# Performance work log

Measured on AMD Instinct MI355X. Metric: run time of the kernel, lower is better.

The kernel has to match this reference:

```python
import jax, jax.numpy as jnp
import numpy as np

N_NODES = 40000
N_EDGES = 640000
D_FEAT = 128
HIDDEN = 128
N_CLASSES = 10
N_GRAPHS = 64


def setup_inputs() -> dict:
    key = jax.random.key(0)
    ks = jax.random.split(key, 8)
    x = jax.random.normal(ks[0], (N_NODES, D_FEAT), dtype=jnp.float32)
    edge_index = jax.random.randint(ks[1], (2, N_EDGES), 0, N_NODES, dtype=jnp.int32)
    batch = jnp.sort(jax.random.randint(ks[2], (N_NODES,), 0, N_GRAPHS, dtype=jnp.int32))
    s1 = 1.0 / np.sqrt(D_FEAT)
    s2 = 1.0 / np.sqrt(HIDDEN)
    W1 = jax.random.normal(ks[3], (D_FEAT, HIDDEN), dtype=jnp.float32) * s1
    b1 = jnp.zeros((HIDDEN,), dtype=jnp.float32)
    W2 = jax.random.normal(ks[4], (HIDDEN, HIDDEN), dtype=jnp.float32) * s2
    b2 = jnp.zeros((HIDDEN,), dtype=jnp.float32)
    lin_w = jax.random.normal(ks[5], (HIDDEN, N_CLASSES), dtype=jnp.float32) * s2
    lin_b = jnp.zeros((N_CLASSES,), dtype=jnp.float32)
    return {"x": x, "edge_index": edge_index, "batch": batch,
            "W1": W1, "b1": b1, "W2": W2, "b2": b2,
            "lin_w": lin_w, "lin_b": lin_b}


def _gcn_conv(x, src, dst, norm, W, b, n_nodes):
    # x' = D^-1/2 (A + I) D^-1/2 (x W) + b ; self-loops already in src/dst/norm
    xw = x @ W                                   # [N, H]
    msg = xw[src] * norm[:, None]                # gather + scale  [E+N, H]
    out = jax.ops.segment_sum(msg, dst, num_segments=n_nodes)  # scatter-add
    return out + b


def reference(x, edge_index, batch, W1, b1, W2, b2, lin_w, lin_b):
    n_nodes = x.shape[0]
    loop = jnp.arange(n_nodes, dtype=edge_index.dtype)
    src = jnp.concatenate([edge_index[0], loop])  # add self-loops (fill=1)
    dst = jnp.concatenate([edge_index[1], loop])
    deg = jax.ops.segment_sum(jnp.ones_like(src, dtype=x.dtype), dst,
                              num_segments=n_nodes)
    dinv = jnp.where(deg > 0, jax.lax.rsqrt(jnp.maximum(deg, 1e-12)), 0.0)
    norm = dinv[src] * dinv[dst]

    h = jax.nn.relu(_gcn_conv(x, src, dst, norm, W1, b1, n_nodes))
    h = jax.nn.relu(_gcn_conv(h, src, dst, norm, W2, b2, n_nodes))

    # global average pooling per graph
    sums = jax.ops.segment_sum(h, batch, num_segments=N_GRAPHS)      # [B, H]
    cnt = jax.ops.segment_sum(jnp.ones((n_nodes,), x.dtype), batch,
                              num_segments=N_GRAPHS)
    pooled = sums / jnp.maximum(cnt, 1.0)[:, None]

    logits = pooled @ lin_w + lin_b                                  # [B, K]
    return logits
```

## Files before the change

kernel.cpp:

```cpp
#include <hip/hip_runtime.h>
#include <stdint.h>

#define N_NODES 40000
#define N_EDGES 640000
#define HID 128
#define NGRAPH 64
#define NCLASS 10
#define CAP 64
#define POISON ((int)0xAAAAAAAAu)
#define ZROW 40000

typedef unsigned short u16;
typedef unsigned char u8;
typedef __attribute__((ext_vector_type(8))) short bf16x8;
typedef __attribute__((ext_vector_type(4))) float f32x4;
typedef __attribute__((ext_vector_type(2))) float f32x2;

static __device__ __forceinline__ u16 f2bf(float f) {
    union { float f; uint32_t i; } v; v.f = f;
    uint32_t u = v.i;
    u = (u + 0x7fff + ((u >> 16) & 1)) >> 16;
    return (u16)u;
}

static __device__ __forceinline__ void acc_row(uint2 p, float* a) {
    f32x2 f01 = __builtin_amdgcn_cvt_pk_f32_fp8((int)p.x, false);
    f32x2 f23 = __builtin_amdgcn_cvt_pk_f32_fp8((int)p.x, true);
    f32x2 f45 = __builtin_amdgcn_cvt_pk_f32_fp8((int)p.y, false);
    f32x2 f67 = __builtin_amdgcn_cvt_pk_f32_fp8((int)p.y, true);
    a[0] += f01[0]; a[1] += f01[1]; a[2] += f23[0]; a[3] += f23[1];
    a[4] += f45[0]; a[5] += f45[1]; a[6] += f67[0]; a[7] += f67[1];
}

static __device__ __forceinline__ void agg_gather_pad(const u8* __restrict__ base,
        const u16* __restrict__ csr, int e, int e1, float* a) {
    int sc[6]; uint2 pc[6];
    #pragma unroll
    for (int u = 0; u < 6; ++u) sc[u] = (int)csr[e + u];
    #pragma unroll
    for (int u = 0; u < 6; ++u) pc[u] = *(const uint2*)(base + (size_t)sc[u] * HID);
    e += 6;
    while (e < e1) {
        int sn[6]; uint2 pn[6];
        #pragma unroll
        for (int u = 0; u < 6; ++u) sn[u] = (int)csr[e + u];
        #pragma unroll
        for (int u = 0; u < 6; ++u) pn[u] = *(const uint2*)(base + (size_t)sn[u] * HID);
        #pragma unroll
        for (int u = 0; u < 6; ++u) acc_row(pc[u], a);
        #pragma unroll
        for (int u = 0; u < 6; ++u) pc[u] = pn[u];
        e += 6;
    }
    #pragma unroll
    for (int u = 0; u < 6; ++u) acc_row(pc[u], a);
}

static __device__ __forceinline__ int padded_deg(int deg) {
    int degp = ((deg + 5) / 6) * 6;
    if (degp < 6) degp = 6;
    if (degp > 60) degp = 60;
    return degp;
}

__launch_bounds__(256)
__global__ void k_fill_wprep(const int* __restrict__ srcs, const int* __restrict__ dsts,
                             int* __restrict__ cursor, u16* __restrict__ csr,
                             const float* __restrict__ W1, const float* __restrict__ W2,
                             u16* __restrict__ wswz1, u16* __restrict__ wswz2) {
    if (blockIdx.x < 2500) {
        int e = blockIdx.x * 256 + threadIdx.x;
        int s = srcs[e], d = dsts[e];
        int old = atomicAdd(&cursor[d], 1);
        int slot = old - POISON;
        if (slot < CAP) csr[(d << 6) + slot] = (u16)s;
    } else {
        int gid = (blockIdx.x - 2500) * 256 + threadIdx.x;
        int idx = gid & 16383;
        const float* W = (gid < 16384) ? W1 : W2;
        u16* o = (gid < 16384) ? wswz1 : wswz2;
        int j = idx & 7;
        int frag = idx >> 3;
        int l = frag & 63;
        int ks = (frag >> 6) & 3;
        int nt = frag >> 8;
        int k = ks * 32 + (l >> 4) * 8 + j;
        int n = nt * 16 + (l & 15);
        o[idx] = f2bf(W[k * HID + n]);
    }
}

__launch_bounds__(256)
__global__ void k_gemm1(const float* __restrict__ x, const u16* __restrict__ wswz1,
                        const int* __restrict__ cursor, u8* __restrict__ z1,
                        u16* __restrict__ csr) {
    __shared__ u16 wlds[16384];
    int t = threadIdx.x;
    if (blockIdx.x >= 625) {
        if (blockIdx.x == 625 && t < 16)
            *(uint2*)(z1 + (size_t)ZROW * HID + t * 8) = make_uint2(0u, 0u);
        int nid = (blockIdx.x - 625) * 256 + t;
        if (nid < N_NODES) {
            int deg = cursor[nid] - POISON;
            int degp = padded_deg(deg);
            for (int s = deg; s < degp; ++s) csr[(nid << 6) + s] = (u16)ZROW;
        }
        return;
    }
    {
        const uint4* s4 = (const uint4*)wswz1;
        uint4* d4 = (uint4*)wlds;
        #pragma unroll
        for (int i = 0; i < 8; ++i) d4[t + 256 * i] = s4[t + 256 * i];
    }
    __syncthreads();
    int lane = t & 63, wv = t >> 6;
    int quad = lane >> 4, m15 = lane & 15;
    int strip = blockIdx.x * 4 + wv;
    int m0 = strip * 16;
    float dv[4];
    #pragma unroll
    for (int r = 0; r < 4; ++r)
        dv[r] = rsqrtf((float)(cursor[m0 + quad * 4 + r] - POISON + 1));
    bf16x8 af[4];
    const float* arow = x + (size_t)(m0 + m15) * HID;
    #pragma unroll
    for (int ks = 0; ks < 4; ++ks) {
        float4 u = *(const float4*)(arow + ks * 32 + quad * 8);
        float4 v = *(const float4*)(arow + ks * 32 + quad * 8 + 4);
        bf16x8 f;
        f[0] = (short)f2bf(u.x); f[1] = (short)f2bf(u.y);
        f[2] = (short)f2bf(u.z); f[3] = (short)f2bf(u.w);
        f[4] = (short)f2bf(v.x); f[5] = (short)f2bf(v.y);
        f[6] = (short)f2bf(v.z); f[7] = (short)f2bf(v.w);
        af[ks] = f;
    }
    #pragma unroll
    for (int nt = 0; nt < 8; ++nt) {
        f32x4 acc = {0.f, 0.f, 0.f, 0.f};
        #pragma unroll
        for (int ks = 0; ks < 4; ++ks) {
            bf16x8 bfr = *(const bf16x8*)(&wlds[((nt * 4 + ks) * 64 + lane) * 8]);
            acc = __builtin_amdgcn_mfma_f32_16x16x32_bf16(af[ks], bfr, acc, 0, 0, 0);
        }
        #pragma unroll
        for (int r = 0; r < 4; ++r) {
            float zc = acc[r] * dv[r];
            int pk = __builtin_amdgcn_cvt_pk_fp8_f32(zc, zc, 0, false);
            z1[(size_t)(m0 + quad * 4 + r) * HID + nt * 16 + m15] = (u8)pk;
        }
    }
}

__launch_bounds__(256, 8)
__global__ void k_agg_gemm(const u8* __restrict__ zin, const int* __restrict__ cursor,
                           const u16* __restrict__ csr, const float* __restrict__ bias,
                           const u16* __restrict__ wswz2, u8* __restrict__ zout) {
    __shared__ u16 htile[16 * 136];
    int t = threadIdx.x;
    if (blockIdx.x == 0 && t < 16)
        *(uint2*)(zout + (size_t)ZROW * HID + t * 8) = make_uint2(0u, 0u);
    int lane = t & 63, wv = t >> 6;
    int q = lane >> 4, sub = lane & 15;
    int i = blockIdx.x * 16 + wv * 4 + q;
    int deg = cursor[i] - POISON;
    int degp = padded_deg(deg);
    float di = rsqrtf((float)(deg + 1));
    const u8* base = zin + (size_t)sub * 8;
    uint2 ps = *(const uint2*)(base + (size_t)i * HID);
    float a[8];
    {
        f32x2 t0 = __builtin_amdgcn_cvt_pk_f32_fp8((int)ps.x, false);
        f32x2 t1 = __builtin_amdgcn_cvt_pk_f32_fp8((int)ps.x, true);
        f32x2 t2 = __builtin_amdgcn_cvt_pk_f32_fp8((int)ps.y, false);
        f32x2 t3 = __builtin_amdgcn_cvt_pk_f32_fp8((int)ps.y, true);
        a[0] = t0[0]; a[1] = t0[1]; a[2] = t1[0]; a[3] = t1[1];
        a[4] = t2[0]; a[5] = t2[1]; a[6] = t3[0]; a[7] = t3[1];
    }
    int e = i << 6;
    agg_gather_pad(base, csr, e, e + degp, a);

    float4 b0 = *(const float4*)(bias + sub * 8);
    float4 b1v = *(const float4*)(bias + sub * 8 + 4);
    float r0 = fmaxf(di * a[0] + b0.x, 0.f),  r1 = fmaxf(di * a[1] + b0.y, 0.f);
    float r2 = fmaxf(di * a[2] + b0.z, 0.f),  r3 = fmaxf(di * a[3] + b0.w, 0.f);
    float r4 = fmaxf(di * a[4] + b1v.x, 0.f), r5 = fmaxf(di * a[5] + b1v.y, 0.f);
    float r6 = fmaxf(di * a[6] + b1v.z, 0.f), r7 = fmaxf(di * a[7] + b1v.w, 0.f);
    int nl = wv * 4 + q;
    uint4 o;
    o.x = (uint32_t)f2bf(r0) | ((uint32_t)f2bf(r1) << 16);
    o.y = (uint32_t)f2bf(r2) | ((uint32_t)f2bf(r3) << 16);
    o.z = (uint32_t)f2bf(r4) | ((uint32_t)f2bf(r5) << 16);
    o.w = (uint32_t)f2bf(r6) | ((uint32_t)f2bf(r7) << 16);
    *(uint4*)(&htile[nl * 136 + sub * 8]) = o;
    __syncthreads();

    int quad = q, m15 = sub;
    bf16x8 af[4];
    #pragma unroll
    for (int ks = 0; ks < 4; ++ks)
        af[ks] = *(const bf16x8*)(&htile[m15 * 136 + ks * 32 + quad * 8]);
    int m0 = blockIdx.x * 16;
    float dv[4];
    #pragma unroll
    for (int r = 0; r < 4; ++r)
        dv[r] = rsqrtf((float)(cursor[m0 + quad * 4 + r] - POISON + 1));
    #pragma unroll
    for (int n2 = 0; n2 < 2; ++n2) {
        int nt = wv * 2 + n2;
        f32x4 acc = {0.f, 0.f, 0.f, 0.f};
        #pragma unroll
        for (int ks = 0; ks < 4; ++ks) {
            bf16x8 bfr = *(const bf16x8*)(wswz2 + ((nt * 4 + ks) * 64 + lane) * 8);
            acc = __builtin_amdgcn_mfma_f32_16x16x32_bf16(af[ks], bfr, acc, 0, 0, 0);
        }
        #pragma unroll
        for (int r = 0; r < 4; ++r) {
            float zc = acc[r] * dv[r];
            int pk = __builtin_amdgcn_cvt_pk_fp8_f32(zc, zc, 0, false);
            zout[(size_t)(m0 + quad * 4 + r) * HID + nt * 16 + m15] = (u8)pk;
        }
    }
}

__launch_bounds__(256, 8)
__global__ void k_agg2pool(const u8* __restrict__ zin, const int* __restrict__ cursor,
                           const u16* __restrict__ csr, const float* __restrict__ bias,
                           const int* __restrict__ batch, float* __restrict__ gpool) {
    __shared__ float hf[16 * 132];
    __shared__ int sbatch[16];
    int t = threadIdx.x;
    int lane = t & 63, wv = t >> 6;
    int q = lane >> 4, sub = lane & 15;
    int i = blockIdx.x * 16 + wv * 4 + q;
    if (t < 16) sbatch[t] = batch[blockIdx.x * 16 + t];
    int deg = cursor[i] - POISON;
    int degp = padded_deg(deg);
    float di = rsqrtf((float)(deg + 1));
    const u8* base = zin + (size_t)sub * 8;
    uint2 ps = *(const uint2*)(base + (size_t)i * HID);
    float a[8];
    {
        f32x2 t0 = __builtin_amdgcn_cvt_pk_f32_fp8((int)ps.x, false);
        f32x2 t1 = __builtin_amdgcn_cvt_pk_f32_fp8((int)ps.x, true);
        f32x2 t2 = __builtin_amdgcn_cvt_pk_f32_fp8((int)ps.y, false);
        f32x2 t3 = __builtin_amdgcn_cvt_pk_f32_fp8((int)ps.y, true);
        a[0] = t0[0]; a[1] = t0[1]; a[2] = t1[0]; a[3] = t1[1];
        a[4] = t2[0]; a[5] = t2[1]; a[6] = t3[0]; a[7] = t3[1];
    }
    int e = i << 6;
    agg_gather_pad(base, csr, e, e + degp, a);

    float4 b0 = *(const float4*)(bias + sub * 8);
    float4 b1v = *(const float4*)(bias + sub * 8 + 4);
    int nl = wv * 4 + q;
    float* hrow = &hf[nl * 132 + sub * 8];
    float4 o0, o1;
    o0.x = fmaxf(di * a[0] + b0.x, 0.f);  o0.y = fmaxf(di * a[1] + b0.y, 0.f);
    o0.z = fmaxf(di * a[2] + b0.z, 0.f);  o0.w = fmaxf(di * a[3] + b0.w, 0.f);
    o1.x = fmaxf(di * a[4] + b1v.x, 0.f); o1.y = fmaxf(di * a[5] + b1v.y, 0.f);
    o1.z = fmaxf(di * a[6] + b1v.z, 0.f); o1.w = fmaxf(di * a[7] + b1v.w, 0.f);
    *(float4*)hrow = o0;
    *(float4*)(hrow + 4) = o1;
    __syncthreads();

    if (t < HID) {
        float s = 0.f;
        int gcur = sbatch[0];
        #pragma unroll
        for (int j = 0; j < 16; ++j) {
            int gj = sbatch[j];
            if (gj != gcur) {
                atomicAdd(&gpool[gcur * HID + t], s);
                s = 0.f;
                gcur = gj;
            }
            s += hf[j * 132 + t];
        }
        atomicAdd(&gpool[gcur * HID + t], s);
    }
}

__launch_bounds__(128)
__global__ void k_pool2(const float* __restrict__ gpool, const int* __restrict__ batch,
                        const float* __restrict__ lin_w, const float* __restrict__ lin_b,
                        float* __restrict__ outp) {
    __shared__ float sh[HID];
    int g = blockIdx.x;
    int t = threadIdx.x;
    int lo = 0, n = N_NODES;
    while (n > 0) { int half = n >> 1; int mid = lo + half;
        if (batch[mid] < g) { lo = mid + 1; n -= half + 1; } else n = half; }
    int hi = lo, n2 = N_NODES - lo;
    while (n2 > 0) { int half = n2 >> 1; int mid = hi + half;
        if (batch[mid] < g + 1) { hi = mid + 1; n2 -= half + 1; } else n2 = half; }
    float c = fmaxf((float)(hi - lo), 1.f);
    sh[t] = gpool[g * HID + t] / c;
    __syncthreads();
    if (t < NCLASS) {
        float a = lin_b[t];
        #pragma unroll 8
        for (int f = 0; f < HID; ++f)
            a += sh[f] * lin_w[f * NCLASS + t];
        outp[g * NCLASS + t] = a;
    }
}

extern "C" void kernel_launch(void* const* d_in, const int* in_sizes, int n_in,
                              void* d_out, int out_size, void* d_ws, size_t ws_size,
                              hipStream_t stream) {
    const float* x    = (const float*)d_in[0];
    const int* eidx   = (const int*)d_in[1];
    const int* batch  = (const int*)d_in[2];
    const float* W1   = (const float*)d_in[3];
    const float* b1   = (const float*)d_in[4];
    const float* W2   = (const float*)d_in[5];
    const float* b2   = (const float*)d_in[6];
    const float* lw   = (const float*)d_in[7];
    const float* lb   = (const float*)d_in[8];
    float* out = (float*)d_out;

    char* ws = (char*)d_ws;
    int*   cursor  = (int*)(ws + 0);
    float* gpool   = (float*)(ws + 160000);
    u16*   csr     = (u16*)(ws + 192768);
    u16*   wswz1   = (u16*)(ws + 5312768);
    u16*   wswz2   = (u16*)(ws + 5345536);
    u8*    bufZ1   = (u8*)(ws + 5378304);
    u8*    bufZ2   = (u8*)(ws + 10498432);

    const int* src = eidx;
    const int* dst = eidx + N_EDGES;

    k_fill_wprep<<<2628, 256, 0, stream>>>(src, dst, cursor, csr, W1, W2, wswz1, wswz2);
    k_gemm1<<<782, 256, 0, stream>>>(x, wswz1, cursor, bufZ1, csr);
    k_agg_gemm<<<2500, 256, 0, stream>>>(bufZ1, cursor, csr, b1,
                                         wswz2, bufZ2);
    k_agg2pool<<<2500, 256, 0, stream>>>(bufZ2, cursor, csr, b2,
                                         batch, gpool);
    k_pool2<<<NGRAPH, 128, 0, stream>>>(gpool, batch, lw, lb, out);
}
```

Measured before the change: 158.4 us.

## Split feature rows into XCD-pinned halves and separate layer-2 aggregation from GEMM

The fp8 node-feature buffers are re-laid out as two 64-byte column halves with separate row ranges. Each aggregation block handles one half, chosen from blockIdx modulo 8, so that four XCDs gather only from one half and their L2 caches hold a smaller working set. The fused layer-1 aggregate+GEMM kernel is split into k_agg1, which writes bf16 h1 to global memory, and a new k_gemm2 that stages W2 in LDS. The aim is better L2 hit rates on the random gathers, at the cost of an extra global round trip for h1, one more launch, and twice as many blocks each doing half the work per row.

```diff
diff --git a/kernel.cpp b/kernel.cpp
--- a/kernel.cpp
+++ b/kernel.cpp
@@ -9,6 +9,7 @@
 #define CAP 64
 #define POISON ((int)0xAAAAAAAAu)
 #define ZROW 40000
+#define RSTRIDE 40001
 
 typedef unsigned short u16;
 typedef unsigned char u8;
@@ -23,37 +24,34 @@
     return (u16)u;
 }
 
-static __device__ __forceinline__ void acc_row(uint2 p, float* a) {
-    f32x2 f01 = __builtin_amdgcn_cvt_pk_f32_fp8((int)p.x, false);
-    f32x2 f23 = __builtin_amdgcn_cvt_pk_f32_fp8((int)p.x, true);
-    f32x2 f45 = __builtin_amdgcn_cvt_pk_f32_fp8((int)p.y, false);
-    f32x2 f67 = __builtin_amdgcn_cvt_pk_f32_fp8((int)p.y, true);
+static __device__ __forceinline__ void acc_row4(uint32_t p, float* a) {
+    f32x2 f01 = __builtin_amdgcn_cvt_pk_f32_fp8((int)p, false);
+    f32x2 f23 = __builtin_amdgcn_cvt_pk_f32_fp8((int)p, true);
     a[0] += f01[0]; a[1] += f01[1]; a[2] += f23[0]; a[3] += f23[1];
-    a[4] += f45[0]; a[5] += f45[1]; a[6] += f67[0]; a[7] += f67[1];
-}
-
-static __device__ __forceinline__ void agg_gather_pad(const u8* __restrict__ base,
+}
+
+static __device__ __forceinline__ void agg_gather_pad4(const u8* __restrict__ lb,
         const u16* __restrict__ csr, int e, int e1, float* a) {
-    int sc[6]; uint2 pc[6];
+    int sc[6]; uint32_t pc[6];
     #pragma unroll
     for (int u = 0; u < 6; ++u) sc[u] = (int)csr[e + u];
     #pragma unroll
-    for (int u = 0; u < 6; ++u) pc[u] = *(const uint2*)(base + (size_t)sc[u] * HID);
+    for (int u = 0; u < 6; ++u) pc[u] = *(const uint32_t*)(lb + (size_t)sc[u] * 64);
     e += 6;
     while (e < e1) {
-        int sn[6]; uint2 pn[6];
+        int sn[6]; uint32_t pn[6];
         #pragma unroll
         for (int u = 0; u < 6; ++u) sn[u] = (int)csr[e + u];
         #pragma unroll
-        for (int u = 0; u < 6; ++u) pn[u] = *(const uint2*)(base + (size_t)sn[u] * HID);
-        #pragma unroll
-        for (int u = 0; u < 6; ++u) acc_row(pc[u], a);
+        for (int u = 0; u < 6; ++u) pn[u] = *(const uint32_t*)(lb + (size_t)sn[u] * 64);
+        #pragma unroll
+        for (int u = 0; u < 6; ++u) acc_row4(pc[u], a);
         #pragma unroll
         for (int u = 0; u < 6; ++u) pc[u] = pn[u];
         e += 6;
     }
     #pragma unroll
-    for (int u = 0; u < 6; ++u) acc_row(pc[u], a);
+    for (int u = 0; u < 6; ++u) acc_row4(pc[u], a);
 }
 
 static __device__ __forceinline__ int padded_deg(int deg) {
@@ -97,8 +95,11 @@
     __shared__ u16 wlds[16384];
     int t = threadIdx.x;
     if (blockIdx.x >= 625) {
-        if (blockIdx.x == 625 && t < 16)
-            *(uint2*)(z1 + (size_t)ZROW * HID + t * 8) = make_uint2(0u, 0u);
+        if (blockIdx.x == 625 && t < 16) {
+            int hh = t >> 3;
+            *(uint2*)(z1 + ((size_t)(hh * RSTRIDE + ZROW)) * 64 + (t & 7) * 8)
+                = make_uint2(0u, 0u);
+        }
         int nid = (blockIdx.x - 625) * 256 + t;
         if (nid < N_NODES) {
             int deg = cursor[nid] - POISON;
@@ -147,78 +148,93 @@
         for (int r = 0; r < 4; ++r) {
             float zc = acc[r] * dv[r];
             int pk = __builtin_amdgcn_cvt_pk_fp8_f32(zc, zc, 0, false);
-            z1[(size_t)(m0 + quad * 4 + r) * HID + nt * 16 + m15] = (u8)pk;
+            int node = m0 + quad * 4 + r;
+            z1[((size_t)((nt >> 2) * RSTRIDE + node)) * 64 + (nt & 3) * 16 + m15] = (u8)pk;
         }
     }
 }
 
 __launch_bounds__(256, 8)
-__global__ void k_agg_gemm(const u8* __restrict__ zin, const int* __restrict__ cursor,
-                           const u16* __restrict__ csr, const float* __restrict__ bias,
-                           const u16* __restrict__ wswz2, u8* __restrict__ zout) {
-    __shared__ u16 htile[16 * 136];
-    int t = threadIdx.x;
-    if (blockIdx.x == 0 && t < 16)
-        *(uint2*)(zout + (size_t)ZROW * HID + t * 8) = make_uint2(0u, 0u);
+__global__ void k_agg1(const u8* __restrict__ zin, const int* __restrict__ cursor,
+                       const u16* __restrict__ csr, const float* __restrict__ bias,
+                       u16* __restrict__ h1) {
+    int t = threadIdx.x;
+    int bid = blockIdx.x;
+    int xcd = bid & 7;
+    int half = xcd >> 2;
+    int s = (bid >> 3) * 4 + (xcd & 3);
     int lane = t & 63, wv = t >> 6;
-    int q = lane >> 4, sub = lane & 15;
-    int i = blockIdx.x * 16 + wv * 4 + q;
+    int q = lane >> 4, L = lane & 15;
+    int i = s * 16 + wv * 4 + q;
     int deg = cursor[i] - POISON;
     int degp = padded_deg(deg);
     float di = rsqrtf((float)(deg + 1));
-    const u8* base = zin + (size_t)sub * 8;
-    uint2 ps = *(const uint2*)(base + (size_t)i * HID);
-    float a[8];
+    const u8* lb = zin + (size_t)(half * RSTRIDE) * 64 + L * 4;
+    uint32_t ps = *(const uint32_t*)(lb + (size_t)i * 64);
+    float a[4];
     {
-        f32x2 t0 = __builtin_amdgcn_cvt_pk_f32_fp8((int)ps.x, false);
-        f32x2 t1 = __builtin_amdgcn_cvt_pk_f32_fp8((int)ps.x, true);
-        f32x2 t2 = __builtin_amdgcn_cvt_pk_f32_fp8((int)ps.y, false);
-        f32x2 t3 = __builtin_amdgcn_cvt_pk_f32_fp8((int)ps.y, true);
-        a[0] = t0[0]; a[1] = t0[1]; a[2] = t1[0]; a[3] = t1[1];
-        a[4] = t2[0]; a[5] = t2[1]; a[6] = t3[0]; a[7] = t3[1];
+        f32x2 f01 = __builtin_amdgcn_cvt_pk_f32_fp8((int)ps, false);
+        f32x2 f23 = __builtin_amdgcn_cvt_pk_f32_fp8((int)ps, true);
+        a[0] = f01[0]; a[1] = f01[1]; a[2] = f23[0]; a[3] = f23[1];
     }
     int e = i << 6;
-    agg_gather_pad(base, csr, e, e + degp, a);
-
-    float4 b0 = *(const float4*)(bias + sub * 8);
-    float4 b1v = *(const float4*)(bias + sub * 8 + 4);
-    float r0 = fmaxf(di * a[0] + b0.x, 0.f),  r1 = fmaxf(di * a[1] + b0.y, 0.f);
-    float r2 = fmaxf(di * a[2] + b0.z, 0.f),  r3 = fmaxf(di * a[3] + b0.w, 0.f);
-    float r4 = fmaxf(di * a[4] + b1v.x, 0.f), r5 = fmaxf(di * a[5] + b1v.y, 0.f);
-    float r6 = fmaxf(di * a[6] + b1v.z, 0.f), r7 = fmaxf(di * a[7] + b1v.w, 0.f);
-    int nl = wv * 4 + q;
-    uint4 o;
+    agg_gather_pad4(lb, csr, e, e + degp, a);
+    float4 b = *(const float4*)(bias + half * 64 + L * 4);
+    float r0 = fmaxf(di * a[0] + b.x, 0.f), r1 = fmaxf(di * a[1] + b.y, 0.f);
+    float r2 = fmaxf(di * a[2] + b.z, 0.f), r3 = fmaxf(di * a[3] + b.w, 0.f);
+    uint2 o;
     o.x = (uint32_t)f2bf(r0) | ((uint32_t)f2bf(r1) << 16);
     o.y = (uint32_t)f2bf(r2) | ((uint32_t)f2bf(r3) << 16);
-    o.z = (uint32_t)f2bf(r4) | ((uint32_t)f2bf(r5) << 16);
-    o.w = (uint32_t)f2bf(r6) | ((uint32_t)f2bf(r7) << 16);
-    *(uint4*)(&htile[nl * 136 + sub * 8]) = o;
+    *(uint2*)(h1 + ((size_t)(half * N_NODES + i)) * 64 + L * 4) = o;
+}
+
+__launch_bounds__(256)
+__global__ void k_gemm2(const u16* __restrict__ h1, const u16* __restrict__ wswz2,
+                        const int* __restrict__ cursor, u8* __restrict__ z2) {
+    __shared__ u16 wlds[16384];
+    int t = threadIdx.x;
+    {
+        const uint4* s4 = (const uint4*)wswz2;
+        uint4* d4 = (uint4*)wlds;
+        #pragma unroll
+        for (int i = 0; i < 8; ++i) d4[t + 256 * i] = s4[t + 256 * i];
+    }
+    if (blockIdx.x == 0 && t < 16) {
+        int hh = t >> 3;
+        *(uint2*)(z2 + ((size_t)(hh * RSTRIDE + ZROW)) * 64 + (t & 7) * 8)
+            = make_uint2(0u, 0u);
+    }
     __syncthreads();
-
-    int quad = q, m15 = sub;
-    bf16x8 af[4];
-    #pragma unroll
-    for (int ks = 0; ks < 4; ++ks)
-        af[ks] = *(const bf16x8*)(&htile[m15 * 136 + ks * 32 + quad * 8]);
-    int m0 = blockIdx.x * 16;
+    int lane = t & 63, wv = t >> 6;
+    int quad = lane >> 4, m15 = lane & 15;
+    int strip = blockIdx.x * 4 + wv;
+    int m0 = strip * 16;
     float dv[4];
     #pragma unroll
     for (int r = 0; r < 4; ++r)
         dv[r] = rsqrtf((float)(cursor[m0 + quad * 4 + r] - POISON + 1));
-    #pragma unroll
-    for (int n2 = 0; n2 < 2; ++n2) {
-        int nt = wv * 2 + n2;
+    bf16x8 af[4];
+    int node = m0 + m15;
+    #pragma unroll
+    for (int ks = 0; ks < 4; ++ks) {
+        int f = ks * 32 + quad * 8;
+        int hh = f >> 6, fo = f & 63;
+        af[ks] = *(const bf16x8*)(h1 + ((size_t)(hh * N_NODES + node)) * 64 + fo);
+    }
+    #pragma unroll
+    for (int nt = 0; nt < 8; ++nt) {
         f32x4 acc = {0.f, 0.f, 0.f, 0.f};
         #pragma unroll
         for (int ks = 0; ks < 4; ++ks) {
-            bf16x8 bfr = *(const bf16x8*)(wswz2 + ((nt * 4 + ks) * 64 + lane) * 8);
+            bf16x8 bfr = *(const bf16x8*)(&wlds[((nt * 4 + ks) * 64 + lane) * 8]);
             acc = __builtin_amdgcn_mfma_f32_16x16x32_bf16(af[ks], bfr, acc, 0, 0, 0);
         }
         #pragma unroll
         for (int r = 0; r < 4; ++r) {
             float zc = acc[r] * dv[r];
             int pk = __builtin_amdgcn_cvt_pk_fp8_f32(zc, zc, 0, false);
-            zout[(size_t)(m0 + quad * 4 + r) * HID + nt * 16 + m15] = (u8)pk;
+            int nd = m0 + quad * 4 + r;
+            z2[((size_t)((nt >> 2) * RSTRIDE + nd)) * 64 + (nt & 3) * 16 + m15] = (u8)pk;
         }
     }
 }
@@ -227,57 +243,54 @@
 __global__ void k_agg2pool(const u8* __restrict__ zin, const int* __restrict__ cursor,
                            const u16* __restrict__ csr, const float* __restrict__ bias,
                            const int* __restrict__ batch, float* __restrict__ gpool) {
-    __shared__ float hf[16 * 132];
+    __shared__ float hf[16 * 68];
     __shared__ int sbatch[16];
     int t = threadIdx.x;
+    int bid = blockIdx.x;
+    int xcd = bid & 7;
+    int half = xcd >> 2;
+    int s = (bid >> 3) * 4 + (xcd & 3);
+    if (t < 16) sbatch[t] = batch[s * 16 + t];
     int lane = t & 63, wv = t >> 6;
-    int q = lane >> 4, sub = lane & 15;
-    int i = blockIdx.x * 16 + wv * 4 + q;
-    if (t < 16) sbatch[t] = batch[blockIdx.x * 16 + t];
+    int q = lane >> 4, L = lane & 15;
+    int i = s * 16 + wv * 4 + q;
     int deg = cursor[i] - POISON;
     int degp = padded_deg(deg);
     float di = rsqrtf((float)(deg + 1));
-    const u8* base = zin + (size_t)sub * 8;
-    uint2 ps = *(const uint2*)(base + (size_t)i * HID);
-    float a[8];
+    const u8* lb = zin + (size_t)(half * RSTRIDE) * 64 + L * 4;
+    uint32_t ps = *(const uint32_t*)(lb + (size_t)i * 64);
+    float a[4];
     {
-        f32x2 t0 = __builtin_amdgcn_cvt_pk_f32_fp8((int)ps.x, false);
-        f32x2 t1 = __builtin_amdgcn_cvt_pk_f32_fp8((int)ps.x, true);
-        f32x2 t2 = __builtin_amdgcn_cvt_pk_f32_fp8((int)ps.y, false);
-        f32x2 t3 = __builtin_amdgcn_cvt_pk_f32_fp8((int)ps.y, true);
-        a[0] = t0[0]; a[1] = t0[1]; a[2] = t1[0]; a[3] = t1[1];
-        a[4] = t2[0]; a[5] = t2[1]; a[6] = t3[0]; a[7] = t3[1];
+        f32x2 f01 = __builtin_amdgcn_cvt_pk_f32_fp8((int)ps, false);
+        f32x2 f23 = __builtin_amdgcn_cvt_pk_f32_fp8((int)ps, true);
+        a[0] = f01[0]; a[1] = f01[1]; a[2] = f23[0]; a[3] = f23[1];
     }
     int e = i << 6;
-    agg_gather_pad(base, csr, e, e + degp, a);
-
-    float4 b0 = *(const float4*)(bias + sub * 8);
-    float4 b1v = *(const float4*)(bias + sub * 8 + 4);
+    agg_gather_pad4(lb, csr, e, e + degp, a);
+    float4 b = *(const float4*)(bias + half * 64 + L * 4);
     int nl = wv * 4 + q;
-    float* hrow = &hf[nl * 132 + sub * 8];
-    float4 o0, o1;
-    o0.x = fmaxf(di * a[0] + b0.x, 0.f);  o0.y = fmaxf(di * a[1] + b0.y, 0.f);
-    o0.z = fmaxf(di * a[2] + b0.z, 0.f);  o0.w = fmaxf(di * a[3] + b0.w, 0.f);
-    o1.x = fmaxf(di * a[4] + b1v.x, 0.f); o1.y = fmaxf(di * a[5] + b1v.y, 0.f);
-    o1.z = fmaxf(di * a[6] + b1v.z, 0.f); o1.w = fmaxf(di * a[7] + b1v.w, 0.f);
-    *(float4*)hrow = o0;
-    *(float4*)(hrow + 4) = o1;
+    float4 o;
+    o.x = fmaxf(di * a[0] + b.x, 0.f);
+    o.y = fmaxf(di * a[1] + b.y, 0.f);
+    o.z = fmaxf(di * a[2] + b.z, 0.f);
+    o.w = fmaxf(di * a[3] + b.w, 0.f);
+    *(float4*)(&hf[nl * 68 + L * 4]) = o;
     __syncthreads();
 
-    if (t < HID) {
-        float s = 0.f;
+    if (t < 64) {
+        float ssum = 0.f;
         int gcur = sbatch[0];
         #pragma unroll
         for (int j = 0; j < 16; ++j) {
             int gj = sbatch[j];
             if (gj != gcur) {
-                atomicAdd(&gpool[gcur * HID + t], s);
-                s = 0.f;
+                atomicAdd(&gpool[gcur * HID + half * 64 + t], ssum);
+                ssum = 0.f;
                 gcur = gj;
             }
-            s += hf[j * 132 + t];
-        }
-        atomicAdd(&gpool[gcur * HID + t], s);
+            ssum += hf[j * 68 + t];
+        }
+        atomicAdd(&gpool[gcur * HID + half * 64 + t], ssum);
     }
 }
 
@@ -327,16 +340,17 @@
     u16*   wswz1   = (u16*)(ws + 5312768);
     u16*   wswz2   = (u16*)(ws + 5345536);
     u8*    bufZ1   = (u8*)(ws + 5378304);
-    u8*    bufZ2   = (u8*)(ws + 10498432);
+    u16*   h1      = (u16*)(ws + 10498432);
+    u8*    bufZ2   = (u8*)(ws + 20738432);
 
     const int* src = eidx;
     const int* dst = eidx + N_EDGES;
 
     k_fill_wprep<<<2628, 256, 0, stream>>>(src, dst, cursor, csr, W1, W2, wswz1, wswz2);
     k_gemm1<<<782, 256, 0, stream>>>(x, wswz1, cursor, bufZ1, csr);
-    k_agg_gemm<<<2500, 256, 0, stream>>>(bufZ1, cursor, csr, b1,
-                                         wswz2, bufZ2);
-    k_agg2pool<<<2500, 256, 0, stream>>>(bufZ2, cursor, csr, b2,
+    k_agg1<<<5000, 256, 0, stream>>>(bufZ1, cursor, csr, b1, h1);
+    k_gemm2<<<625, 256, 0, stream>>>(h1, wswz2, cursor, bufZ2);
+    k_agg2pool<<<5000, 256, 0, stream>>>(bufZ2, cursor, csr, b2,
                                          batch, gpool);
     k_pool2<<<NGRAPH, 128, 0, stream>>>(gpool, batch, lw, lb, out);
 }
```

Measured after the change: 162.7 us. +2.7%, slower.

## Partition edges into destination buckets before building CSR

Applied to the files above, without the earlier changes.

Replaces the direct per-edge atomic CSR fill with two passes. The first bins edges by destination block of 512 nodes using shared-memory counters plus one global atomic per bucket per block. The second kernel walks each bucket and does the per-destination atomics and CSR writes, so those accesses stay within a localized address range. This aims to reduce scattered global atomics and cache misses, at the cost of an extra kernel launch and an intermediate buffer round trip. It relies on the workspace being poison-initialized for gbcur, and on BCAP being large enough for each bucket.

```diff
diff --git a/kernel.cpp b/kernel.cpp
--- a/kernel.cpp
+++ b/kernel.cpp
@@ -9,6 +9,8 @@
 #define CAP 64
 #define POISON ((int)0xAAAAAAAAu)
 #define ZROW 40000
+#define NBKT 80
+#define BCAP 12288
 
 typedef unsigned short u16;
 typedef unsigned char u8;
@@ -64,17 +66,11 @@
 }
 
 __launch_bounds__(256)
-__global__ void k_fill_wprep(const int* __restrict__ srcs, const int* __restrict__ dsts,
-                             int* __restrict__ cursor, u16* __restrict__ csr,
+__global__ void k_part_wprep(const int* __restrict__ srcs, const int* __restrict__ dsts,
+                             int* __restrict__ gbcur, uint32_t* __restrict__ barr,
                              const float* __restrict__ W1, const float* __restrict__ W2,
                              u16* __restrict__ wswz1, u16* __restrict__ wswz2) {
-    if (blockIdx.x < 2500) {
-        int e = blockIdx.x * 256 + threadIdx.x;
-        int s = srcs[e], d = dsts[e];
-        int old = atomicAdd(&cursor[d], 1);
-        int slot = old - POISON;
-        if (slot < CAP) csr[(d << 6) + slot] = (u16)s;
-    } else {
+    if (blockIdx.x >= 2500) {
         int gid = (blockIdx.x - 2500) * 256 + threadIdx.x;
         int idx = gid & 16383;
         const float* W = (gid < 16384) ? W1 : W2;
@@ -87,6 +83,35 @@
         int k = ks * 32 + (l >> 4) * 8 + j;
         int n = nt * 16 + (l & 15);
         o[idx] = f2bf(W[k * HID + n]);
+        return;
+    }
+    __shared__ int lcnt[NBKT];
+    __shared__ int lbase[NBKT];
+    int t = threadIdx.x;
+    if (t < NBKT) lcnt[t] = 0;
+    __syncthreads();
+    int e = blockIdx.x * 256 + t;
+    int s = srcs[e], d = dsts[e];
+    int b = d >> 9;
+    int myrank = atomicAdd(&lcnt[b], 1);
+    __syncthreads();
+    if (t < NBKT && lcnt[t] > 0)
+        lbase[t] = atomicAdd(&gbcur[t], lcnt[t]) - POISON;
+    __syncthreads();
+    barr[b * BCAP + lbase[b] + myrank] = ((uint32_t)d << 16) | (uint32_t)s;
+}
+
+__launch_bounds__(256)
+__global__ void k_fill2(const uint32_t* __restrict__ barr, const int* __restrict__ gbcur,
+                        int* __restrict__ cursor, u16* __restrict__ csr) {
+    int b = blockIdx.x >> 2, sub = blockIdx.x & 3;
+    int n = gbcur[b] - POISON;
+    const uint32_t* ba = barr + (size_t)b * BCAP;
+    for (int i = sub * 256 + threadIdx.x; i < n; i += 1024) {
+        uint32_t p = ba[i];
+        int d = (int)(p >> 16), s = (int)(p & 0xFFFFu);
+        int slot = atomicAdd(&cursor[d], 1) - POISON;
+        if (slot < CAP) csr[(d << 6) + slot] = (u16)s;
     }
 }
 
@@ -321,18 +346,21 @@
     float* out = (float*)d_out;
 
     char* ws = (char*)d_ws;
-    int*   cursor  = (int*)(ws + 0);
-    float* gpool   = (float*)(ws + 160000);
-    u16*   csr     = (u16*)(ws + 192768);
-    u16*   wswz1   = (u16*)(ws + 5312768);
-    u16*   wswz2   = (u16*)(ws + 5345536);
-    u8*    bufZ1   = (u8*)(ws + 5378304);
-    u8*    bufZ2   = (u8*)(ws + 10498432);
+    int*      cursor = (int*)(ws + 0);
+    float*    gpool  = (float*)(ws + 160000);
+    u16*      csr    = (u16*)(ws + 192768);
+    u16*      wswz1  = (u16*)(ws + 5312768);
+    u16*      wswz2  = (u16*)(ws + 5345536);
+    u8*       bufZ1  = (u8*)(ws + 5378304);
+    u8*       bufZ2  = (u8*)(ws + 10498432);
+    int*      gbcur  = (int*)(ws + 15618560);
+    uint32_t* barr   = (uint32_t*)(ws + 15618880);
 
     const int* src = eidx;
     const int* dst = eidx + N_EDGES;
 
-    k_fill_wprep<<<2628, 256, 0, stream>>>(src, dst, cursor, csr, W1, W2, wswz1, wswz2);
+    k_part_wprep<<<2628, 256, 0, stream>>>(src, dst, gbcur, barr, W1, W2, wswz1, wswz2);
+    k_fill2<<<4 * NBKT, 256, 0, stream>>>(barr, gbcur, cursor, csr);
     k_gemm1<<<782, 256, 0, stream>>>(x, wswz1, cursor, bufZ1, csr);
     k_agg_gemm<<<2500, 256, 0, stream>>>(bufZ1, cursor, csr, b1,
                                          wswz2, bufZ2);
```

Result: slower. 195.9 us (+23.7%).
